# Performance work log

Hardware: AMD Instinct MI355X
Metric: run time of the kernel (lower is better)

## Reference

```python
import jax, jax.numpy as jnp
import numpy as np

# ---- hyperparameters matching init_kwargs / input_specs ----
K = 16          # max neighbors kept per node (avg degree)
ALPHA = 0.5     # FGW trade-off (POT default used in the repo)
FW_ITERS = 5    # Frank-Wolfe (conditional-gradient) outer iterations
SK_ITERS = 20   # log-domain Sinkhorn inner iterations
REG = 0.1       # entropic regularization for the inner OT solve
NEG = -1e9      # "log(0)" for masked (padded) neighborhood slots


def build_neighbors(edge_index, n, k):
    """Fixed-size (padded) neighbor table from a COO edge list."""
    src, dst = edge_index[0], edge_index[1]
    order = jnp.argsort(src)
    s_src, s_dst = src[order], dst[order]
    ids = jnp.arange(n)
    start = jnp.searchsorted(s_src, ids)
    end = jnp.searchsorted(s_src, ids, side='right')
    cnt = jnp.minimum(end - start, k)                       # [n]
    pos = start[:, None] + jnp.arange(k)[None, :]           # [n,k]
    valid = jnp.arange(k)[None, :] < cnt[:, None]           # [n,k]
    nbrs = s_dst[jnp.clip(pos, 0, s_src.shape[0] - 1)]      # [n,k]
    return nbrs, valid


def reference(x, edge_index, templates, templates_features):
    n, d = x.shape
    nbrs, valid = build_neighbors(edge_index, n, K)
    # local node set per node: self + up to K neighbors -> K1 = K+1 slots
    S = jnp.concatenate([jnp.arange(n)[:, None], nbrs], axis=1)            # [n,K1]
    mask = jnp.concatenate([jnp.ones((n, 1), bool), valid], axis=1)        # [n,K1]
    mf = mask.astype(x.dtype)

    # local subgraph adjacency: A[i,a,b] = 1 iff edge S[i,a] -> S[i,b]
    nbrs_of = nbrs[S]                                                      # [n,K1,K]
    valid_of = valid[S]
    eq = (nbrs_of[:, :, None, :] == S[:, None, :, None]) & valid_of[:, :, None, :]
    C1 = eq.any(-1).astype(x.dtype) * mf[:, :, None] * mf[:, None, :]      # [n,K1,K1]

    F1 = x[S] * mf[:, :, None]                                             # [n,K1,d]
    F2 = templates_features                                                # [T,t,d]
    # squared-euclidean feature cost M[i,T,a,b] = ||F1[i,a]-F2[T,b]||^2
    M = (jnp.sum(F1 ** 2, -1)[:, None, :, None]
         + jnp.sum(F2 ** 2, -1)[None, :, None, :]
         - 2.0 * jnp.einsum('nad,tbd->ntab', F1, F2))                      # [n,T,K1,t]

    cnt1 = mf.sum(1)                                                       # [n] (>=1: self)
    p = mf / cnt1[:, None]                                                 # [n,K1] uniform masked
    t_n = templates.shape[1]
    q = jnp.full((t_n,), 1.0 / t_n, x.dtype)
    C2 = templates                                                         # [T,t,t]

    # GW square-loss decomposition (POT): tens = constC - 2*C1 @ T @ C2^T
    constC = (jnp.einsum('nab,nb->na', C1 ** 2, p)[:, None, :, None]
              + jnp.einsum('tab,b->ta', C2 ** 2, q)[None, :, None, :])     # [n,T,K1,t]

    def tens_of(T):
        tmp = jnp.einsum('nac,ntcd->ntad', C1, T)
        cross = jnp.einsum('ntad,tbd->ntab', tmp, C2)
        return constC - 2.0 * cross

    logp = jnp.where(mask, -jnp.log(cnt1)[:, None], NEG)[:, None, :]       # [n,1,K1]
    logq = -jnp.log(jnp.asarray(t_n, x.dtype))                             # scalar

    def sinkhorn(G):
        logK = -G / REG                                                    # [n,T,K1,t]
        f = jnp.zeros(G.shape[:3], G.dtype)
        g = jnp.zeros(G.shape[:2] + (t_n,), G.dtype)
        def body(_, fg):
            f, g = fg
            g = logq - jax.nn.logsumexp(logK + f[..., :, None], axis=-2)
            f = logp - jax.nn.logsumexp(logK + g[..., None, :], axis=-1)
            return (f, g)
        f, g = jax.lax.fori_loop(0, SK_ITERS, body, (f, g))
        return jnp.exp(f[..., :, None] + g[..., None, :] + logK)

    T0 = p[:, None, :, None] * q[None, None, None, :]                      # [n,1->T,K1,t]
    T0 = jnp.broadcast_to(T0, M.shape)

    def fw_step(T, k):
        tens = tens_of(T)
        G = (1.0 - ALPHA) * M + 2.0 * ALPHA * tens                         # FGW gradient
        Tn = sinkhorn(G)                                                   # linear-min oracle
        gamma = 2.0 / (k + 2.0)
        return (1.0 - gamma) * T + gamma * Tn, None

    T, _ = jax.lax.scan(fw_step, T0, jnp.arange(FW_ITERS, dtype=x.dtype))

    tens = tens_of(T)
    dist = ((1.0 - ALPHA) * jnp.sum(M * T, axis=(-2, -1))
            + ALPHA * jnp.sum(tens * T, axis=(-2, -1)))                    # [n,T]
    return dist


def setup_inputs() -> dict:
    key = jax.random.key(0)
    k1, k2, k3, k4 = jax.random.split(key, 4)
    n, d, e = 10000, 128, 160000
    n_T, t_n = 10, 10
    x = jax.random.normal(k1, (n, d), jnp.float32)
    edge_index = jax.random.randint(k2, (2, e), 0, n, jnp.int64)
    templates = jax.random.uniform(k3, (n_T, t_n, t_n), jnp.float32)
    templates_features = jax.random.normal(k4, (n_T, t_n, d), jnp.float32)
    return {"x": x, "edge_index": edge_index,
            "templates": templates, "templates_features": templates_features}
```

## Files before the change

### kernel.cpp

```cpp
#include <hip/hip_runtime.h>
#include <math.h>

#define NNODE 10000
#define NEDGE 160000
#define KNB   16
#define K1    17
#define NT    10
#define TN    10
#define DF    128
#define CAP   64
#define NEG_BIG (-1e9f)

#define LOGQ2      (-3.32192809489f)
#define KB_SCALE   (-14.4269504089f)
#define CR_SCALE   (28.8539008178f)
#define G_SCALE    (-0.069314718056f)
#define LN2        0.69314718056f
#define TINYF      1e-30f

#if defined(__has_builtin)
#if __has_builtin(__builtin_amdgcn_exp2f)
#define EXP2F(x) __builtin_amdgcn_exp2f(x)
#endif
#if __has_builtin(__builtin_amdgcn_rcpf)
#define RCPF(x) __builtin_amdgcn_rcpf(x)
#endif
#endif
#ifndef EXP2F
#define EXP2F(x) __expf((x) * LN2)
#endif
#ifndef RCPF
#define RCPF(x) (1.0f / (x))
#endif
#define LOG2F(x) __log2f(x)

#define CBAR() asm volatile("" ::: "memory")

__device__ __forceinline__ float2 pk_add(float2 a, float2 b) { return make_float2(a.x + b.x, a.y + b.y); }
__device__ __forceinline__ float2 pk_sub(float2 a, float2 b) { return make_float2(a.x - b.x, a.y - b.y); }
__device__ __forceinline__ float2 pk_mul(float2 a, float2 b) { return make_float2(a.x * b.x, a.y * b.y); }
__device__ __forceinline__ float2 pk_max(float2 a, float2 b) { return make_float2(fmaxf(a.x, b.x), fmaxf(a.y, b.y)); }
__device__ __forceinline__ float2 pk_fma(float2 a, float2 b, float2 c) { return make_float2(fmaf(a.x, b.x, c.x), fmaf(a.y, b.y, c.y)); }
__device__ __forceinline__ float2 pk_exp2(float2 a) { return make_float2(EXP2F(a.x), EXP2F(a.y)); }
__device__ __forceinline__ float clamp120(float x) { return fminf(120.f, fmaxf(-120.f, x)); }

__device__ __forceinline__ int detect_wide(const int* ei) {
  int z = 0;
#pragma unroll
  for (int i = 0; i < 32; ++i) z |= ei[2 * i + 1];
  return z == 0;
}

__global__ void __launch_bounds__(256) k_prep(const int* __restrict__ ei,
                                              int* cnt, int* ebuf,
                                              const float* __restrict__ x,
                                              const float* __restrict__ tf,
                                              const float* __restrict__ tmpl,
                                              float* __restrict__ dots,
                                              float* __restrict__ nxv,
                                              float* __restrict__ nF2,
                                              float* __restrict__ Bq) {
  __shared__ float xs[64][DF];
  const int tid = threadIdx.x;
  if (blockIdx.x < 625) {
    int e = blockIdx.x * 256 + tid;
    int wide = detect_wide(ei);
    int s = wide ? ei[2 * e] : ei[e];
    int pos = atomicAdd(&cnt[s], 1);
    if (pos < CAP) ebuf[s * CAP + pos] = e;
    return;
  }
  const int db = blockIdx.x - 625;
  if (db == 0 && tid < NT * TN) {
    const float* fp = tf + (size_t)tid * DF;
    float s = 0.f;
    for (int d = 0; d < DF; ++d) { float v = fp[d]; s += v * v; }
    nF2[tid] = s;
    const float* cp = tmpl + (size_t)tid * TN;
    float s2 = 0.f;
    for (int c = 0; c < TN; ++c) { float v = cp[c]; s2 += v * v; }
    Bq[tid] = 0.1f * s2;
  }
  const int nb = db * 64;
  const int nvalid = (NNODE - nb) < 64 ? (NNODE - nb) : 64;
  {
    const float4* xg = (const float4*)(x + (size_t)nb * DF);
    float4* xl = (float4*)&xs[0][0];
    for (int i = tid; i < nvalid * (DF / 4); i += 256) xl[i] = xg[i];
  }
  __syncthreads();
  for (int o = tid; o < nvalid * (NT * TN); o += 256) {
    int n = o / (NT * TN);
    int tb = o - n * (NT * TN);
    const float4* fp = (const float4*)(tf + (size_t)tb * DF);
    const float4* xp = (const float4*)&xs[n][0];
    float s = 0.f;
#pragma unroll
    for (int d = 0; d < DF / 4; ++d) {
      float4 a = xp[d], f = fp[d];
      s += a.x * f.x + a.y * f.y + a.z * f.z + a.w * f.w;
    }
    dots[(size_t)(nb + n) * (NT * TN) + tb] = s;
  }
  if (tid < nvalid) {
    const float4* xp = (const float4*)&xs[tid][0];
    float s = 0.f;
#pragma unroll
    for (int d = 0; d < DF / 4; ++d) {
      float4 a = xp[d];
      s += a.x * a.x + a.y * a.y + a.z * a.z + a.w * a.w;
    }
    nxv[nb + tid] = s;
  }
}

__global__ void k_select(const int* ei, const int* cnt, const int* ebuf,
                         int* nbrs, int* kcnt, int* Sg) {
  int i = blockIdx.x * blockDim.x + threadIdx.x;
  if (i >= NNODE) return;
  int wide = detect_wide(ei);
  int c = cnt[i]; c = c > CAP ? CAP : c;
  int best[KNB];
  int m = 0;
  for (int j = 0; j < c; ++j) {
    int e = ebuf[i * CAP + j];
    if (m < KNB) {
      int p = m++;
      while (p > 0 && best[p - 1] > e) { best[p] = best[p - 1]; --p; }
      best[p] = e;
    } else if (e < best[KNB - 1]) {
      int p = KNB - 1;
      while (p > 0 && best[p - 1] > e) { best[p] = best[p - 1]; --p; }
      best[p] = e;
    }
  }
  kcnt[i] = m;
  Sg[i * K1 + 0] = i;
  for (int j = 0; j < KNB; ++j) {
    int v = 0;
    if (j < m) {
      int e = best[j];
      v = wide ? ei[2 * (NEDGE + e)] : ei[NEDGE + e];
    }
    nbrs[i * KNB + j] = v;
    Sg[i * K1 + 1 + j] = v;
  }
}

__global__ void __launch_bounds__(256) k_c1b(const int* __restrict__ nbrs,
                                             const int* __restrict__ kcnt,
                                             const int* __restrict__ Sg,
                                             unsigned int* __restrict__ bitsG,
                                             float* __restrict__ Ag) {
  int idx = blockIdx.x * 256 + threadIdx.x;
  if (idx >= NNODE * K1) return;
  int i = idx / K1;
  int a = idx - i * K1;
  int kc = kcnt[i];
  unsigned int vmask = (kc >= KNB) ? 0x1FFFFu : ((2u << kc) - 1u);
  unsigned int bits = 0;
  bool va = (a == 0) || (a - 1 < kc);
  if (va) {
    int S[K1];
#pragma unroll
    for (int b = 0; b < K1; ++b) S[b] = Sg[i * K1 + b];
    int u = S[a];
    int ku = kcnt[u];
    const int* np = nbrs + (size_t)u * KNB;
    for (int j = 0; j < ku; ++j) {
      int w = np[j];
#pragma unroll
      for (int b = 0; b < K1; ++b) bits |= (S[b] == w) ? (1u << b) : 0u;
    }
    bits &= vmask;
  }
  bitsG[idx] = bits;
  Ag[idx] = (float)__popc(bits) / (float)(1 + kc);
}

__global__ void __launch_bounds__(128, 3) k_main(
    const float* __restrict__ tmpl,
    const int* __restrict__ kcnt, const int* __restrict__ Sg,
    const unsigned int* __restrict__ bitsG, const float* __restrict__ Ag,
    const float* __restrict__ dots, const float* __restrict__ nxv,
    const float* __restrict__ nF2, const float* __restrict__ Bq,
    float* __restrict__ out)
{
  __shared__ float KT[2 * 5 * 204 + 48];
  __shared__ float fL[2][5][20];
  __shared__ float gL[2][5][12];
  __shared__ float uL[2][5][20];
  __shared__ float wL[2][5][12];
  __shared__ float accL[2][5][TN];

  const int wv = threadIdx.x >> 6;
  const int lane = threadIdx.x & 63;
  int p = lane / 10;
  const int b = lane - p * 10;
  const bool act = (p < 5);
  if (!act) p = 4;
  const int node = blockIdx.x;
  const int t = wv * 5 + p;
  const int tb = t * TN + b;
  float* KTp = &KT[(wv * 5 + p) * 204];

  const int kc = kcnt[node];
  const float cnt1 = (float)(1 + kc);
  const float inv_cnt1 = 1.f / cnt1;
  const float logp2v = -LOG2F(cnt1);
  const float lp2_r0 = ((b == 0) || (b - 1 < kc)) ? logp2v : NEG_BIG;
  const float lp2_r1 = ((9 + b) < kc) ? logp2v : NEG_BIG;

  float2 c2v[5];
  {
    const float2* cp = (const float2*)(tmpl + (size_t)tb * TN);
#pragma unroll
    for (int j = 0; j < 5; ++j) c2v[j] = cp[j];
  }
  const float Bb = Bq[tb];
  const float nf2b = nF2[tb];

  float2 Kb2v[8]; float kb16;
  float2 Tp2[10];
#pragma unroll
  for (int j = 0; j < 10; ++j) Tp2[j] = make_float2(0.f, 0.f);
  unsigned int bw[K1];
#pragma unroll
  for (int a = 0; a < K1; ++a) {
    bool va = (a == 0) || (a - 1 < kc);
    int sa = Sg[node * K1 + a];
    float Ma = (va ? (nxv[sa] - 2.f * dots[(size_t)sa * (NT * TN) + tb]) : 0.f) + nf2b;
    float base = 0.5f * Ma + Ag[node * K1 + a] + Bb;
    float kv = KB_SCALE * base;
    float tv = va ? (inv_cnt1 * 0.1f) : 0.f;
    if (a == 16) kb16 = kv;
    else if (a & 1) Kb2v[a >> 1].y = kv;
    else Kb2v[a >> 1].x = kv;
    if (a < 10) Tp2[a].x = tv; else Tp2[a - 10].y = tv;
    bw[a] = bitsG[node * K1 + a];
  }

  float2 Kc2v[8]; float k16 = 0.f;
  float2 Kr0v[5], Kr1v[5];
  float2 gr[5];
  float g2 = 0.f, fr0 = 0.f, fr1 = 0.f;

#pragma unroll 1
  for (int k = 0; k < 6; ++k) {
    if (act) {
#pragma unroll
      for (int a = 0; a < K1; ++a)
        KTp[a * 12 + b] = (a < 10) ? Tp2[a].x : Tp2[a - 10].y;
    }
    CBAR();
    float R[K1];
#pragma unroll
    for (int c = 0; c < K1; ++c) {
      const float* row = &KTp[c * 12];
      float4 u0 = *(const float4*)row;
      float4 u1 = *(const float4*)(row + 4);
      float2 u2 = *(const float2*)(row + 8);
      float2 accA = pk_mul(make_float2(u0.x, u0.y), c2v[0]);
      accA = pk_fma(make_float2(u0.z, u0.w), c2v[1], accA);
      float2 accB = pk_mul(make_float2(u1.x, u1.y), c2v[2]);
      accB = pk_fma(make_float2(u1.z, u1.w), c2v[3], accB);
      accA = pk_fma(u2, c2v[4], accA);
      accA = pk_add(accA, accB);
      R[c] = accA.x + accA.y;
    }
#pragma unroll
    for (int a = 0; a < K1; ++a) {
      float cr = 0.f;
      unsigned int m = bw[a];
      if (m) {
#pragma unroll
        for (int c = 0; c < K1; ++c)
          if (m & (1u << c)) cr += R[c];
      }
      float base = (a == 16) ? kb16 : ((a & 1) ? Kb2v[a >> 1].y : Kb2v[a >> 1].x);
      float val = base + CR_SCALE * cr;
      if (a == 16) k16 = val;
      else if (a & 1) Kc2v[a >> 1].y = val;
      else Kc2v[a >> 1].x = val;
    }

    if (k == 5) {
      float acc = 0.f;
#pragma unroll
      for (int a = 0; a < K1; ++a) {
        bool va = (a == 0) || (a - 1 < kc);
        int sa = Sg[node * K1 + a];
        float Ma = (va ? (nxv[sa] - 2.f * dots[(size_t)sa * (NT * TN) + tb]) : 0.f) + nf2b;
        float kcv = (a == 16) ? k16 : ((a & 1) ? Kc2v[a >> 1].y : Kc2v[a >> 1].x);
        float tpv = (a < 10) ? Tp2[a].x : Tp2[a - 10].y;
        acc += tpv * (0.25f * Ma + 0.5f * (G_SCALE * kcv));
      }
      if (act) accL[wv][p][b] = acc;
      CBAR();
      if (lane < 5) {
        float s = 0.f;
#pragma unroll
        for (int j = 0; j < TN; ++j) s += accL[wv][lane][j];
        out[node * NT + wv * 5 + lane] = s;
      }
      return;
    }

    CBAR();
    if (act) {
#pragma unroll
      for (int a = 0; a < 16; ++a) KTp[a * 12 + b] = (a & 1) ? Kc2v[a >> 1].y : Kc2v[a >> 1].x;
      KTp[16 * 12 + b] = k16;
    }
    CBAR();
    {
      const float* r0 = &KTp[b * 12];
      float4 u0 = *(const float4*)r0;
      float4 u1 = *(const float4*)(r0 + 4);
      float2 u2 = *(const float2*)(r0 + 8);
      Kr0v[0] = make_float2(u0.x, u0.y); Kr0v[1] = make_float2(u0.z, u0.w);
      Kr0v[2] = make_float2(u1.x, u1.y); Kr0v[3] = make_float2(u1.z, u1.w);
      Kr0v[4] = u2;
      const float* r1 = &KTp[(10 + b) * 12];
      float4 w0 = *(const float4*)r1;
      float4 w1 = *(const float4*)(r1 + 4);
      float2 w2 = *(const float2*)(r1 + 8);
      Kr1v[0] = make_float2(w0.x, w0.y); Kr1v[1] = make_float2(w0.z, w0.w);
      Kr1v[2] = make_float2(w1.x, w1.y); Kr1v[3] = make_float2(w1.z, w1.w);
      Kr1v[4] = w2;
    }

#pragma unroll 1
    for (int it = 0; it < 2; ++it) {
      float2 v[8]; float v16;
      if (it == 0) {
#pragma unroll
        for (int i = 0; i < 8; ++i) v[i] = Kc2v[i];
        v16 = k16;
      } else {
        float4 f0 = *(const float4*)&fL[wv][p][0];
        float4 f1 = *(const float4*)&fL[wv][p][4];
        float4 f2 = *(const float4*)&fL[wv][p][8];
        float4 f3 = *(const float4*)&fL[wv][p][12];
        float fx = fL[wv][p][16];
        v[0] = pk_add(Kc2v[0], make_float2(f0.x, f0.y));
        v[1] = pk_add(Kc2v[1], make_float2(f0.z, f0.w));
        v[2] = pk_add(Kc2v[2], make_float2(f1.x, f1.y));
        v[3] = pk_add(Kc2v[3], make_float2(f1.z, f1.w));
        v[4] = pk_add(Kc2v[4], make_float2(f2.x, f2.y));
        v[5] = pk_add(Kc2v[5], make_float2(f2.z, f2.w));
        v[6] = pk_add(Kc2v[6], make_float2(f3.x, f3.y));
        v[7] = pk_add(Kc2v[7], make_float2(f3.z, f3.w));
        v16 = k16 + fx;
      }
      float2 m01 = pk_max(pk_max(v[0], v[1]), pk_max(v[2], v[3]));
      float2 m23 = pk_max(pk_max(v[4], v[5]), pk_max(v[6], v[7]));
      float2 mm = pk_max(m01, m23);
      float mx = fmaxf(fmaxf(mm.x, mm.y), v16);
      float2 mxb = make_float2(mx, mx);
      float2 ssA = pk_exp2(pk_sub(v[0], mxb));
      ssA = pk_add(ssA, pk_exp2(pk_sub(v[1], mxb)));
      ssA = pk_add(ssA, pk_exp2(pk_sub(v[2], mxb)));
      ssA = pk_add(ssA, pk_exp2(pk_sub(v[3], mxb)));
      float2 ssB = pk_exp2(pk_sub(v[4], mxb));
      ssB = pk_add(ssB, pk_exp2(pk_sub(v[5], mxb)));
      ssB = pk_add(ssB, pk_exp2(pk_sub(v[6], mxb)));
      ssB = pk_add(ssB, pk_exp2(pk_sub(v[7], mxb)));
      float2 ss = pk_add(ssA, ssB);
      float s = ss.x + ss.y + EXP2F(v16 - mx);
      g2 = LOGQ2 - mx - LOG2F(s);
      if (act) gL[wv][p][b] = g2;
      CBAR();
      {
        float4 g0 = *(const float4*)&gL[wv][p][0];
        float4 g1 = *(const float4*)&gL[wv][p][4];
        float2 gx = *(const float2*)&gL[wv][p][8];
        gr[0] = make_float2(g0.x, g0.y); gr[1] = make_float2(g0.z, g0.w);
        gr[2] = make_float2(g1.x, g1.y); gr[3] = make_float2(g1.z, g1.w);
        gr[4] = gx;
      }
      float2 w0[5], w1[5];
#pragma unroll
      for (int j = 0; j < 5; ++j) w0[j] = pk_add(Kr0v[j], gr[j]);
#pragma unroll
      for (int j = 0; j < 5; ++j) w1[j] = pk_add(Kr1v[j], gr[j]);
      float2 a01 = pk_max(pk_max(w0[0], w0[1]), pk_max(w0[2], w0[3]));
      a01 = pk_max(a01, w0[4]);
      float mxa = fmaxf(a01.x, a01.y);
      float2 b01 = pk_max(pk_max(w1[0], w1[1]), pk_max(w1[2], w1[3]));
      b01 = pk_max(b01, w1[4]);
      float mxb2 = fmaxf(b01.x, b01.y);
      float2 mab = make_float2(mxa, mxa);
      float2 mbb = make_float2(mxb2, mxb2);
      float2 sx = pk_exp2(pk_sub(w0[0], mab));
      sx = pk_add(sx, pk_exp2(pk_sub(w0[1], mab)));
      sx = pk_add(sx, pk_exp2(pk_sub(w0[2], mab)));
      sx = pk_add(sx, pk_exp2(pk_sub(w0[3], mab)));
      sx = pk_add(sx, pk_exp2(pk_sub(w0[4], mab)));
      float2 sy = pk_exp2(pk_sub(w1[0], mbb));
      sy = pk_add(sy, pk_exp2(pk_sub(w1[1], mbb)));
      sy = pk_add(sy, pk_exp2(pk_sub(w1[2], mbb)));
      sy = pk_add(sy, pk_exp2(pk_sub(w1[3], mbb)));
      sy = pk_add(sy, pk_exp2(pk_sub(w1[4], mbb)));
      fr0 = lp2_r0 - mxa - LOG2F(sx.x + sx.y);
      fr1 = lp2_r1 - mxb2 - LOG2F(sy.x + sy.y);
      if (act) {
        fL[wv][p][b] = fr0;
        if (b < 7) fL[wv][p][10 + b] = fr1;
      }
      CBAR();
    }

    float2 Kcs2[10];
    float P00, P01, Q0;
    float2 Krs01[10];
    {
      float4 F0 = *(const float4*)&fL[wv][p][0];
      float4 F1 = *(const float4*)&fL[wv][p][4];
      float4 F2 = *(const float4*)&fL[wv][p][8];
      float4 F3 = *(const float4*)&fL[wv][p][12];
      float f16v = fL[wv][p][16];
      float fs[K1];
      fs[0] = F0.x; fs[1] = F0.y; fs[2] = F0.z; fs[3] = F0.w;
      fs[4] = F1.x; fs[5] = F1.y; fs[6] = F1.z; fs[7] = F1.w;
      fs[8] = F2.x; fs[9] = F2.y; fs[10] = F2.z; fs[11] = F2.w;
      fs[12] = F3.x; fs[13] = F3.y; fs[14] = F3.z; fs[15] = F3.w;
      fs[16] = f16v;
      float qs[K1];
#pragma unroll
      for (int a = 0; a < K1; ++a) {
        float kcv = (a == 16) ? k16 : ((a & 1) ? Kc2v[a >> 1].y : Kc2v[a >> 1].x);
        qs[a] = kcv + fs[a];
      }
      float sigma = qs[0];
#pragma unroll
      for (int a = 1; a < K1; ++a) sigma = fmaxf(sigma, qs[a]);
#pragma unroll
      for (int j = 0; j < 10; ++j) {
        float kx = EXP2F(qs[j] - sigma);
        float ky = (j < 7) ? EXP2F(qs[10 + j] - sigma) : 0.f;
        Kcs2[j] = make_float2(kx, ky);
      }
      Q0 = EXP2F(clamp120(LOGQ2 - sigma - g2));
      float2 a0[5], a1[5];
#pragma unroll
      for (int j = 0; j < 5; ++j) a0[j] = pk_add(Kr0v[j], gr[j]);
#pragma unroll
      for (int j = 0; j < 5; ++j) a1[j] = pk_add(Kr1v[j], gr[j]);
      float2 r0m = pk_max(pk_max(a0[0], a0[1]), pk_max(a0[2], a0[3]));
      r0m = pk_max(r0m, a0[4]);
      float rho0 = fmaxf(r0m.x, r0m.y);
      float2 r1m = pk_max(pk_max(a1[0], a1[1]), pk_max(a1[2], a1[3]));
      r1m = pk_max(r1m, a1[4]);
      float rho1 = fmaxf(r1m.x, r1m.y);
#pragma unroll
      for (int j = 0; j < 5; ++j) {
        Krs01[2 * j]     = make_float2(EXP2F(a0[j].x - rho0), EXP2F(a1[j].x - rho1));
        Krs01[2 * j + 1] = make_float2(EXP2F(a0[j].y - rho0), EXP2F(a1[j].y - rho1));
      }
      P00 = EXP2F(clamp120((lp2_r0 - rho0) - fr0));
      P01 = EXP2F(clamp120((lp2_r1 - rho1) - fr1));
    }

    float Slast, t0, t1;
    {
      float2 SA = pk_add(pk_add(Kcs2[0], Kcs2[1]), pk_add(Kcs2[2], Kcs2[3]));
      float2 SB = pk_add(pk_add(Kcs2[4], Kcs2[5]), pk_add(Kcs2[6], Kcs2[7]));
      float2 S2 = pk_add(pk_add(SA, SB), pk_add(Kcs2[8], Kcs2[9]));
      float S = fmaxf(S2.x + S2.y, TINYF);
      Slast = S;
      float wb = Q0 * RCPF(S);
      if (act) wL[wv][p][b] = wb;
      CBAR();
      float4 W0 = *(const float4*)&wL[wv][p][0];
      float4 W1 = *(const float4*)&wL[wv][p][4];
      float2 W2 = *(const float2*)&wL[wv][p][8];
      float2 tA = pk_mul(Krs01[0], make_float2(W0.x, W0.x));
      tA = pk_fma(Krs01[1], make_float2(W0.y, W0.y), tA);
      tA = pk_fma(Krs01[2], make_float2(W0.z, W0.z), tA);
      tA = pk_fma(Krs01[3], make_float2(W0.w, W0.w), tA);
      tA = pk_fma(Krs01[4], make_float2(W1.x, W1.x), tA);
      float2 tB = pk_mul(Krs01[5], make_float2(W1.y, W1.y));
      tB = pk_fma(Krs01[6], make_float2(W1.z, W1.z), tB);
      tB = pk_fma(Krs01[7], make_float2(W1.w, W1.w), tB);
      tB = pk_fma(Krs01[8], make_float2(W2.x, W2.x), tB);
      tB = pk_fma(Krs01[9], make_float2(W2.y, W2.y), tB);
      float2 t01 = pk_add(tA, tB);
      t0 = t01.x; t1 = t01.y;
    }
#pragma unroll 1
    for (int it = 0; it < 17; ++it) {
      float u0 = P00 * RCPF(fmaxf(t0, TINYF));
      float u1 = P01 * RCPF(fmaxf(t1, TINYF));
      if (act) *(float2*)&uL[wv][p][2 * b] = make_float2(u0, u1);
      CBAR();
      float4 U0 = *(const float4*)&uL[wv][p][0];
      float4 U1 = *(const float4*)&uL[wv][p][4];
      float4 U2 = *(const float4*)&uL[wv][p][8];
      float4 U3 = *(const float4*)&uL[wv][p][12];
      float4 U4 = *(const float4*)&uL[wv][p][16];
      float2 SA = pk_mul(Kcs2[0], make_float2(U0.x, U0.y));
      SA = pk_fma(Kcs2[1], make_float2(U0.z, U0.w), SA);
      SA = pk_fma(Kcs2[2], make_float2(U1.x, U1.y), SA);
      SA = pk_fma(Kcs2[3], make_float2(U1.z, U1.w), SA);
      SA = pk_fma(Kcs2[4], make_float2(U2.x, U2.y), SA);
      float2 SB = pk_mul(Kcs2[5], make_float2(U2.z, U2.w));
      SB = pk_fma(Kcs2[6], make_float2(U3.x, U3.y), SB);
      SB = pk_fma(Kcs2[7], make_float2(U3.z, U3.w), SB);
      SB = pk_fma(Kcs2[8], make_float2(U4.x, U4.y), SB);
      SB = pk_fma(Kcs2[9], make_float2(U4.z, U4.w), SB);
      float2 S2 = pk_add(SA, SB);
      float S = fmaxf(S2.x + S2.y, TINYF);
      Slast = S;
      float wb = Q0 * RCPF(S);
      if (act) wL[wv][p][b] = wb;
      CBAR();
      float4 W0 = *(const float4*)&wL[wv][p][0];
      float4 W1 = *(const float4*)&wL[wv][p][4];
      float2 W2 = *(const float2*)&wL[wv][p][8];
      float2 tA = pk_mul(Krs01[0], make_float2(W0.x, W0.x));
      tA = pk_fma(Krs01[1], make_float2(W0.y, W0.y), tA);
      tA = pk_fma(Krs01[2], make_float2(W0.z, W0.z), tA);
      tA = pk_fma(Krs01[3], make_float2(W0.w, W0.w), tA);
      tA = pk_fma(Krs01[4], make_float2(W1.x, W1.x), tA);
      float2 tB = pk_mul(Krs01[5], make_float2(W1.y, W1.y));
      tB = pk_fma(Krs01[6], make_float2(W1.z, W1.z), tB);
      tB = pk_fma(Krs01[7], make_float2(W1.w, W1.w), tB);
      tB = pk_fma(Krs01[8], make_float2(W2.x, W2.x), tB);
      tB = pk_fma(Krs01[9], make_float2(W2.y, W2.y), tB);
      float2 t01 = pk_add(tA, tB);
      t0 = t01.x; t1 = t01.y;
    }

    {
      float u0 = P00 * RCPF(fmaxf(t0, TINYF));
      float u1 = P01 * RCPF(fmaxf(t1, TINYF));
      if (act) *(float2*)&uL[wv][p][2 * b] = make_float2(u0, u1);
      CBAR();
      float4 U0 = *(const float4*)&uL[wv][p][0];
      float4 U1 = *(const float4*)&uL[wv][p][4];
      float4 U2 = *(const float4*)&uL[wv][p][8];
      float4 U3 = *(const float4*)&uL[wv][p][12];
      float4 U4 = *(const float4*)&uL[wv][p][16];
      const float gam = 2.f / ((float)k + 2.f);
      const float gs = gam * 0.1f * RCPF(Slast);
      const float om = 1.f - gam;
      const float2 omb = make_float2(om, om);
      const float2 gsb = make_float2(gs, gs);
      float2 uu[10];
      uu[0] = make_float2(U0.x, U0.y); uu[1] = make_float2(U0.z, U0.w);
      uu[2] = make_float2(U1.x, U1.y); uu[3] = make_float2(U1.z, U1.w);
      uu[4] = make_float2(U2.x, U2.y); uu[5] = make_float2(U2.z, U2.w);
      uu[6] = make_float2(U3.x, U3.y); uu[7] = make_float2(U3.z, U3.w);
      uu[8] = make_float2(U4.x, U4.y); uu[9] = make_float2(U4.z, U4.w);
#pragma unroll
      for (int j = 0; j < 10; ++j)
        Tp2[j] = pk_fma(omb, Tp2[j], pk_mul(gsb, pk_mul(Kcs2[j], uu[j])));
    }
  }
}

extern "C" void kernel_launch(void* const* d_in, const int* in_sizes, int n_in,
                              void* d_out, int out_size, void* d_ws, size_t ws_size,
                              hipStream_t stream) {
  const float* x    = (const float*)d_in[0];
  const int*   ei   = (const int*)d_in[1];
  const float* tmpl = (const float*)d_in[2];
  const float* tf   = (const float*)d_in[3];
  float* out = (float*)d_out;

  int* cnt  = (int*)d_ws;
  int* ebuf = cnt + NNODE;
  int* nbrs = ebuf + (size_t)NNODE * CAP;
  int* kcnt = nbrs + (size_t)NNODE * KNB;
  int* Sg   = kcnt + NNODE;
  unsigned int* bits = (unsigned int*)(Sg + (size_t)NNODE * K1);
  float* Ag   = (float*)(bits + (size_t)NNODE * K1);
  float* dots = Ag + (size_t)NNODE * K1;
  float* nxv  = dots + (size_t)NNODE * (NT * TN);
  float* nF2  = nxv + NNODE;
  float* Bq   = nF2 + NT * TN;

  hipMemsetAsync(cnt, 0, NNODE * sizeof(int), stream);
  k_prep<<<625 + (NNODE + 63) / 64, 256, 0, stream>>>(ei, cnt, ebuf, x, tf, tmpl,
                                                      dots, nxv, nF2, Bq);
  k_select<<<(NNODE + 255) / 256, 256, 0, stream>>>(ei, cnt, ebuf, nbrs, kcnt, Sg);
  k_c1b<<<(NNODE * K1 + 255) / 256, 256, 0, stream>>>(nbrs, kcnt, Sg, bits, Ag);
  k_main<<<NNODE, 128, 0, stream>>>(tmpl, kcnt, Sg, bits, Ag, dots, nxv, nF2, Bq, out);
}
```

Baseline: 597.4 us.

## Fuse local adjacency bitmask build into main kernel and transpose edge buffer

Removes the separate k_c1b kernel. Each main-kernel wave now builds the local subgraph adjacency bitmasks itself, with lanes 0-16 each scanning one neighbor list, then broadcasts them via readlane and derives the row degree term from popcount. This drops a launch and the global bits/Ag round trip, but both waves of each block redo the same scan. The edge bucket buffer is also switched to a slot-major layout so k_select's per-thread reads are coalesced across nodes.

```diff
diff --git a/kernel.cpp b/kernel.cpp
--- a/kernel.cpp
+++ b/kernel.cpp
@@ -67,7 +67,7 @@
     int wide = detect_wide(ei);
     int s = wide ? ei[2 * e] : ei[e];
     int pos = atomicAdd(&cnt[s], 1);
-    if (pos < CAP) ebuf[s * CAP + pos] = e;
+    if (pos < CAP) ebuf[pos * NNODE + s] = e;
     return;
   }
   const int db = blockIdx.x - 625;
@@ -123,7 +123,7 @@
   int best[KNB];
   int m = 0;
   for (int j = 0; j < c; ++j) {
-    int e = ebuf[i * CAP + j];
+    int e = ebuf[j * NNODE + i];
     if (m < KNB) {
       int p = m++;
       while (p > 0 && best[p - 1] > e) { best[p] = best[p - 1]; --p; }
@@ -147,41 +147,10 @@
   }
 }
 
-__global__ void __launch_bounds__(256) k_c1b(const int* __restrict__ nbrs,
-                                             const int* __restrict__ kcnt,
-                                             const int* __restrict__ Sg,
-                                             unsigned int* __restrict__ bitsG,
-                                             float* __restrict__ Ag) {
-  int idx = blockIdx.x * 256 + threadIdx.x;
-  if (idx >= NNODE * K1) return;
-  int i = idx / K1;
-  int a = idx - i * K1;
-  int kc = kcnt[i];
-  unsigned int vmask = (kc >= KNB) ? 0x1FFFFu : ((2u << kc) - 1u);
-  unsigned int bits = 0;
-  bool va = (a == 0) || (a - 1 < kc);
-  if (va) {
-    int S[K1];
-#pragma unroll
-    for (int b = 0; b < K1; ++b) S[b] = Sg[i * K1 + b];
-    int u = S[a];
-    int ku = kcnt[u];
-    const int* np = nbrs + (size_t)u * KNB;
-    for (int j = 0; j < ku; ++j) {
-      int w = np[j];
-#pragma unroll
-      for (int b = 0; b < K1; ++b) bits |= (S[b] == w) ? (1u << b) : 0u;
-    }
-    bits &= vmask;
-  }
-  bitsG[idx] = bits;
-  Ag[idx] = (float)__popc(bits) / (float)(1 + kc);
-}
-
 __global__ void __launch_bounds__(128, 3) k_main(
     const float* __restrict__ tmpl,
     const int* __restrict__ kcnt, const int* __restrict__ Sg,
-    const unsigned int* __restrict__ bitsG, const float* __restrict__ Ag,
+    const int* __restrict__ nbrs,
     const float* __restrict__ dots, const float* __restrict__ nxv,
     const float* __restrict__ nF2, const float* __restrict__ Bq,
     float* __restrict__ out)
@@ -211,6 +180,31 @@
   const float lp2_r0 = ((b == 0) || (b - 1 < kc)) ? logp2v : NEG_BIG;
   const float lp2_r1 = ((9 + b) < kc) ? logp2v : NEG_BIG;
 
+  int S_arr[K1];
+#pragma unroll
+  for (int a = 0; a < K1; ++a) S_arr[a] = Sg[node * K1 + a];
+
+  const unsigned int vmask = (kc >= KNB) ? 0x1FFFFu : ((2u << kc) - 1u);
+  unsigned int mybits = 0;
+  if (lane < K1) {
+    bool va = (lane == 0) || (lane - 1 < kc);
+    if (va) {
+      int u = S_arr[lane];
+      int ku = kcnt[u];
+      const int* np = nbrs + (size_t)u * KNB;
+      for (int j = 0; j < ku; ++j) {
+        int w = np[j];
+#pragma unroll
+        for (int c = 0; c < K1; ++c) mybits |= (S_arr[c] == w) ? (1u << c) : 0u;
+      }
+      mybits &= vmask;
+    }
+  }
+  unsigned int bw[K1];
+#pragma unroll
+  for (int a = 0; a < K1; ++a)
+    bw[a] = (unsigned int)__builtin_amdgcn_readlane((int)mybits, a);
+
   float2 c2v[5];
   {
     const float2* cp = (const float2*)(tmpl + (size_t)tb * TN);
@@ -224,20 +218,19 @@
   float2 Tp2[10];
 #pragma unroll
   for (int j = 0; j < 10; ++j) Tp2[j] = make_float2(0.f, 0.f);
-  unsigned int bw[K1];
 #pragma unroll
   for (int a = 0; a < K1; ++a) {
     bool va = (a == 0) || (a - 1 < kc);
-    int sa = Sg[node * K1 + a];
+    int sa = S_arr[a];
     float Ma = (va ? (nxv[sa] - 2.f * dots[(size_t)sa * (NT * TN) + tb]) : 0.f) + nf2b;
-    float base = 0.5f * Ma + Ag[node * K1 + a] + Bb;
+    float ag = (float)__popc(bw[a]) * inv_cnt1;
+    float base = 0.5f * Ma + ag + Bb;
     float kv = KB_SCALE * base;
     float tv = va ? (inv_cnt1 * 0.1f) : 0.f;
     if (a == 16) kb16 = kv;
     else if (a & 1) Kb2v[a >> 1].y = kv;
     else Kb2v[a >> 1].x = kv;
     if (a < 10) Tp2[a].x = tv; else Tp2[a - 10].y = tv;
-    bw[a] = bitsG[node * K1 + a];
   }
 
   float2 Kc2v[8]; float k16 = 0.f;
@@ -289,7 +282,7 @@
 #pragma unroll
       for (int a = 0; a < K1; ++a) {
         bool va = (a == 0) || (a - 1 < kc);
-        int sa = Sg[node * K1 + a];
+        int sa = S_arr[a];
         float Ma = (va ? (nxv[sa] - 2.f * dots[(size_t)sa * (NT * TN) + tb]) : 0.f) + nf2b;
         float kcv = (a == 16) ? k16 : ((a & 1) ? Kc2v[a >> 1].y : Kc2v[a >> 1].x);
         float tpv = (a < 10) ? Tp2[a].x : Tp2[a - 10].y;
@@ -574,9 +567,7 @@
   int* nbrs = ebuf + (size_t)NNODE * CAP;
   int* kcnt = nbrs + (size_t)NNODE * KNB;
   int* Sg   = kcnt + NNODE;
-  unsigned int* bits = (unsigned int*)(Sg + (size_t)NNODE * K1);
-  float* Ag   = (float*)(bits + (size_t)NNODE * K1);
-  float* dots = Ag + (size_t)NNODE * K1;
+  float* dots = (float*)(Sg + (size_t)NNODE * K1);
   float* nxv  = dots + (size_t)NNODE * (NT * TN);
   float* nF2  = nxv + NNODE;
   float* Bq   = nF2 + NT * TN;
@@ -585,6 +576,5 @@
   k_prep<<<625 + (NNODE + 63) / 64, 256, 0, stream>>>(ei, cnt, ebuf, x, tf, tmpl,
                                                       dots, nxv, nF2, Bq);
   k_select<<<(NNODE + 255) / 256, 256, 0, stream>>>(ei, cnt, ebuf, nbrs, kcnt, Sg);
-  k_c1b<<<(NNODE * K1 + 255) / 256, 256, 0, stream>>>(nbrs, kcnt, Sg, bits, Ag);
-  k_main<<<NNODE, 128, 0, stream>>>(tmpl, kcnt, Sg, bits, Ag, dots, nxv, nF2, Bq, out);
+  k_main<<<NNODE, 128, 0, stream>>>(tmpl, kcnt, Sg, nbrs, dots, nxv, nF2, Bq, out);
 }
```

New measurement: 631.3 us. +5.7%, slower.
